# Performance work log

Measured on AMD Instinct MI355X. Metric: run time of the kernel, lower is better.

The kernel has to match this reference:

```python
import jax, jax.numpy as jnp
import numpy as np

H = 4          # heads (both HGTConv and MHA)
LN_EPS = 1e-5
ALPHA = 0.1


def _ln(x, g, b):
    m = x.mean(-1, keepdims=True)
    v = ((x - m) ** 2).mean(-1, keepdims=True)
    return (x - m) * jax.lax.rsqrt(v + LN_EPS) * g + b


def _kqv(x, Wk, bk, Wq, bq, Wv, bv, D):
    N = x.shape[0]
    k = (x @ Wk.T + bk).reshape(N, H, D)
    q = (x @ Wq.T + bq).reshape(N, H, D)
    v = (x @ Wv.T + bv).reshape(N, H, D)
    return k, q, v


def _hgt_edge(q_dst, k_src, v_src, a_rel, m_rel, p_rel, src, dst, n_dst):
    """PyG HGTConv message passing for one edge type: relation-transform,
    per-dst-node softmax, weighted scatter-sum."""
    D = q_dst.shape[-1]
    k = jnp.einsum('nhd,hde->nhe', k_src, a_rel)   # [N_src,H,D]
    v = jnp.einsum('nhd,hde->nhe', v_src, m_rel)
    logit = (q_dst[dst] * k[src]).sum(-1) * p_rel / np.sqrt(D)   # [E,H]
    mx = jax.ops.segment_max(logit, dst, num_segments=n_dst)
    e = jnp.exp(logit - mx[dst])
    s = jax.ops.segment_sum(e, dst, num_segments=n_dst)
    a = e / (s[dst] + 1e-16)
    return jax.ops.segment_sum(v[src] * a[..., None], dst, num_segments=n_dst)  # [N_dst,H,D]


def _hgt_out(agg, x, Wout, bout, skip):
    N, dim = x.shape
    o = jax.nn.gelu(agg.reshape(N, dim), approximate=False) @ Wout.T + bout
    a = jax.nn.sigmoid(skip)
    return a * o + (1.0 - a) * x


def _mha(x, Wi, bi, Wo, bo):
    # self-attention over all entities as a single sequence (batch=1)
    N, dim = x.shape
    D = dim // H
    q, k, v = jnp.split(x @ Wi.T + bi, 3, axis=-1)
    q = q.reshape(N, H, D).transpose(1, 0, 2)
    k = k.reshape(N, H, D).transpose(1, 0, 2)
    v = v.reshape(N, H, D).transpose(1, 0, 2)
    att = jax.nn.softmax(jnp.einsum('hnd,hmd->hnm', q, k) / np.sqrt(D), axis=-1)
    o = jnp.einsum('hnm,hmd->hnd', att, v).transpose(1, 0, 2).reshape(N, dim)
    return o @ Wo.T + bo


def _forward(x_entity, x_passage, query_emb,
             Wk_ent, bk_ent, Wq_ent, bq_ent, Wv_ent, bv_ent, Wout_ent, bout_ent, skip_ent,
             Wk_psg, bk_psg, Wq_psg, bq_psg, Wv_psg, bv_psg, Wout_psg, bout_psg, skip_psg,
             a_e2p, m_e2p, p_e2p, a_p2e, m_p2e, p_p2e,
             mha_in_w, mha_in_b, mha_out_w, mha_out_b,
             ln_ent_g, ln_ent_b, ln_psg_g, ln_psg_b,
             w1, b1, w2, b2,
             e2p_src, e2p_dst, p2e_src, p2e_dst):
    N_e, dim = x_entity.shape
    N_p = x_passage.shape[0]
    D = dim // H
    # ---- HGTConv ----
    k_e, q_e, v_e = _kqv(x_entity, Wk_ent, bk_ent, Wq_ent, bq_ent, Wv_ent, bv_ent, D)
    k_p, q_p, v_p = _kqv(x_passage, Wk_psg, bk_psg, Wq_psg, bq_psg, Wv_psg, bv_psg, D)
    agg_p = _hgt_edge(q_p, k_e, v_e, a_e2p, m_e2p, p_e2p, e2p_src, e2p_dst, N_p)
    agg_e = _hgt_edge(q_e, k_p, v_p, a_p2e, m_p2e, p_p2e, p2e_src, p2e_dst, N_e)
    h_ent = _hgt_out(agg_e, x_entity, Wout_ent, bout_ent, skip_ent)
    h_psg = _hgt_out(agg_p, x_passage, Wout_psg, bout_psg, skip_psg)
    # ---- global entity attention + residual mix + LN ----
    h_glob = _mha(h_ent, mha_in_w, mha_in_b, mha_out_w, mha_out_b)
    h_ent = _ln((1.0 - ALPHA) * h_ent + ALPHA * h_glob, ln_ent_g, ln_ent_b)
    # ---- gather-scale-scatter entity -> passage (kernel target) ----
    q = query_emb.reshape(-1)
    rel = jax.nn.sigmoid(h_ent @ q)                          # [N_e]
    w_ent = h_ent[e2p_src] * rel[e2p_src][:, None]           # gather + scale
    ctx = jax.ops.segment_sum(w_ent, e2p_dst, num_segments=N_p)  # scatter-add
    h_psg = _ln(h_psg + ctx, ln_psg_g, ln_psg_b)
    # ---- scoring head ----
    feats = jnp.concatenate([h_psg, jnp.broadcast_to(q, (N_p, dim))], axis=-1)
    scores = (jax.nn.relu(feats @ w1.T + b1) @ w2.T + b2).squeeze(-1)
    return scores


def setup_inputs() -> dict:
    key = jax.random.key(0)
    N_E, N_P, DIM, NE = 4096, 4096, 256, 262144
    D = DIM // H
    ks = iter(jax.random.split(key, 64))
    def rn(shape, s=1.0):
        return jax.random.normal(next(ks), shape, jnp.float32) * s
    w = 0.05
    inp = {
        'x_entity': rn((N_E, DIM)),
        'x_passage': rn((N_P, DIM)),
        'query_emb': rn((DIM,)),
    }
    for t in ('ent', 'psg'):
        inp['Wk_' + t] = rn((DIM, DIM), w); inp['bk_' + t] = jnp.zeros((DIM,))
        inp['Wq_' + t] = rn((DIM, DIM), w); inp['bq_' + t] = jnp.zeros((DIM,))
        inp['Wv_' + t] = rn((DIM, DIM), w); inp['bv_' + t] = jnp.zeros((DIM,))
        inp['Wout_' + t] = rn((DIM, DIM), w); inp['bout_' + t] = jnp.zeros((DIM,))
        inp['skip_' + t] = jnp.ones(())
    for e in ('e2p', 'p2e'):
        inp['a_' + e] = rn((H, D, D), w)
        inp['m_' + e] = rn((H, D, D), w)
        inp['p_' + e] = jnp.ones((H,))
    inp['mha_in_w'] = rn((3 * DIM, DIM), w); inp['mha_in_b'] = jnp.zeros((3 * DIM,))
    inp['mha_out_w'] = rn((DIM, DIM), w); inp['mha_out_b'] = jnp.zeros((DIM,))
    inp['ln_ent_g'] = jnp.ones((DIM,)); inp['ln_ent_b'] = jnp.zeros((DIM,))
    inp['ln_psg_g'] = jnp.ones((DIM,)); inp['ln_psg_b'] = jnp.zeros((DIM,))
    inp['w1'] = rn((DIM, 2 * DIM), w); inp['b1'] = jnp.zeros((DIM,))
    inp['w2'] = rn((1, DIM), w); inp['b2'] = jnp.zeros((1,))
    inp['e2p_src'] = jax.random.randint(next(ks), (NE,), 0, N_E, jnp.int32)
    inp['e2p_dst'] = jax.random.randint(next(ks), (NE,), 0, N_P, jnp.int32)
    inp['p2e_src'] = jax.random.randint(next(ks), (NE,), 0, N_P, jnp.int32)
    inp['p2e_dst'] = jax.random.randint(next(ks), (NE,), 0, N_E, jnp.int32)
    return inp


def reference(x_entity, x_passage, query_emb,
              Wk_ent, bk_ent, Wq_ent, bq_ent, Wv_ent, bv_ent, Wout_ent, bout_ent, skip_ent,
              Wk_psg, bk_psg, Wq_psg, bq_psg, Wv_psg, bv_psg, Wout_psg, bout_psg, skip_psg,
              a_e2p, m_e2p, p_e2p, a_p2e, m_p2e, p_p2e,
              mha_in_w, mha_in_b, mha_out_w, mha_out_b,
              ln_ent_g, ln_ent_b, ln_psg_g, ln_psg_b,
              w1, b1, w2, b2,
              e2p_src, e2p_dst, p2e_src, p2e_dst):
    return _forward(x_entity, x_passage, query_emb,
                    Wk_ent, bk_ent, Wq_ent, bq_ent, Wv_ent, bv_ent, Wout_ent, bout_ent, skip_ent,
                    Wk_psg, bk_psg, Wq_psg, bq_psg, Wv_psg, bv_psg, Wout_psg, bout_psg, skip_psg,
                    a_e2p, m_e2p, p_e2p, a_p2e, m_p2e, p_p2e,
                    mha_in_w, mha_in_b, mha_out_w, mha_out_b,
                    ln_ent_g, ln_ent_b, ln_psg_g, ln_psg_b,
                    w1, b1, w2, b2,
                    e2p_src, e2p_dst, p2e_src, p2e_dst)
```

## Files before the change

### kernel.cpp

```cpp
#include <hip/hip_runtime.h>
#include <hip/hip_bf16.h>
#include <math.h>

#define DIM 256
#define NHEAD 4
#define HD 64
#define MSPLIT 8

typedef __attribute__((ext_vector_type(8))) short short8b;
typedef __attribute__((ext_vector_type(4))) float f32x4;
typedef __attribute__((ext_vector_type(16))) float f32x16;
typedef __attribute__((ext_vector_type(2))) unsigned int uint2v;

union B8 { uint4 u; short8b v; };

__device__ __forceinline__ float sigmoidf_(float x) { return 1.0f / (1.0f + __expf(-x)); }
__device__ __forceinline__ float geluf_(float x) {
    return 0.5f * x * (1.0f + erff(x * 0.70710678118654752440f));
}
__device__ __forceinline__ float wave_sum64(float v) {
    v += __shfl_xor(v, 32); v += __shfl_xor(v, 16); v += __shfl_xor(v, 8);
    v += __shfl_xor(v, 4);  v += __shfl_xor(v, 2);  v += __shfl_xor(v, 1);
    return v;
}
__device__ __forceinline__ unsigned short f2bf(float f) {
    union { float f; unsigned int u; } a; a.f = f;
    unsigned int u = a.u;
    unsigned int r = (u + 0x7FFFu + ((u >> 16) & 1u)) >> 16;
    return (unsigned short)r;
}
__device__ __forceinline__ unsigned int cvtpk_(float lo, float hi) {
    unsigned int r;
    asm("v_cvt_pk_bf16_f32 %0, %1, %2" : "=v"(r) : "v"(lo), "v"(hi));
    return r;
}
__device__ __forceinline__ uint2v plswap_(unsigned int a, unsigned int b) {
    return __builtin_amdgcn_permlane32_swap(a, b, false, false);
}

template<int DO_GELU>
__launch_bounds__(256)
__global__ void cvt_bf16_kernel(const float* __restrict__ src,
                                unsigned short* __restrict__ dst, int n8)
{
    const int i = blockIdx.x * 256 + threadIdx.x;
    if (i >= n8) return;
    float4 a = reinterpret_cast<const float4*>(src)[2 * i];
    float4 b = reinterpret_cast<const float4*>(src)[2 * i + 1];
    if (DO_GELU) {
        a.x = geluf_(a.x); a.y = geluf_(a.y); a.z = geluf_(a.z); a.w = geluf_(a.w);
        b.x = geluf_(b.x); b.y = geluf_(b.y); b.z = geluf_(b.z); b.w = geluf_(b.w);
    }
    ushort4 lo = {f2bf(a.x), f2bf(a.y), f2bf(a.z), f2bf(a.w)};
    ushort4 hi = {f2bf(b.x), f2bf(b.y), f2bf(b.z), f2bf(b.w)};
    reinterpret_cast<ushort4*>(dst)[2 * i] = lo;
    reinterpret_cast<ushort4*>(dst)[2 * i + 1] = hi;
}

__launch_bounds__(256)
__global__ void cvt_w_kernel(const float* __restrict__ W0, const float* __restrict__ W1,
                             const float* __restrict__ W2, const float* __restrict__ W3,
                             const float* __restrict__ W4, const float* __restrict__ W5,
                             const float* __restrict__ W6, const float* __restrict__ W7,
                             const float* __restrict__ W8, const float* __restrict__ W9,
                             const float* __restrict__ W10, const float* __restrict__ W11,
                             unsigned short* __restrict__ arena)
{
    const float* s;
    switch (blockIdx.y) {
        case 0: s = W0; break;  case 1: s = W1; break;  case 2: s = W2; break;
        case 3: s = W3; break;  case 4: s = W4; break;  case 5: s = W5; break;
        case 6: s = W6; break;  case 7: s = W7; break;  case 8: s = W8; break;
        case 9: s = W9; break;  case 10: s = W10; break; default: s = W11; break;
    }
    const int i = blockIdx.x * 256 + threadIdx.x;
    unsigned short* dst = arena + (size_t)blockIdx.y * 65536;
    float4 a = reinterpret_cast<const float4*>(s)[2 * i];
    float4 b = reinterpret_cast<const float4*>(s)[2 * i + 1];
    ushort4 lo = {f2bf(a.x), f2bf(a.y), f2bf(a.z), f2bf(a.w)};
    ushort4 hi = {f2bf(b.x), f2bf(b.y), f2bf(b.z), f2bf(b.w)};
    reinterpret_cast<ushort4*>(dst)[2 * i] = lo;
    reinterpret_cast<ushort4*>(dst)[2 * i + 1] = hi;
}

template<int OUT_MODE, int WF32, int WBF>
__launch_bounds__(256)
__global__ void bgemm_kernel(const unsigned short* __restrict__ Abf,
                             const unsigned short* __restrict__ W0b,
                             const unsigned short* __restrict__ W1b,
                             const unsigned short* __restrict__ W2b,
                             const float* __restrict__ B0, const float* __restrict__ B1,
                             const float* __restrict__ B2,
                             float* __restrict__ C, int ldc,
                             unsigned short* __restrict__ Cbf, int ldcb,
                             const float* __restrict__ xres,
                             const float* __restrict__ skipv)
{
    const int t = threadIdx.x;
    const int lane = t & 63;
    const int wid = t >> 6;
    const int col16 = lane & 15;
    const int oct = lane >> 4;
    const int r0 = blockIdx.y * 64 + wid * 16;
    const int c0 = blockIdx.x * 64;
    const int widx = c0 >> 8;
    const unsigned short* W = (widx == 0) ? W0b : (widx == 1 ? W1b : W2b);
    const float* Bv = (widx == 0) ? B0 : (widx == 1 ? B1 : B2);
    const int cw = c0 & 255;

    const unsigned short* aptr = Abf + (size_t)(r0 + col16) * 256 + oct * 8;
    const unsigned short* wptr = W + (size_t)(cw + col16) * 256 + oct * 8;

    f32x4 acc0 = {0,0,0,0}, acc1 = {0,0,0,0}, acc2 = {0,0,0,0}, acc3 = {0,0,0,0};
#pragma unroll
    for (int k0 = 0; k0 < 256; k0 += 32) {
        B8 af, w0, w1, w2, w3;
        af.u = *reinterpret_cast<const uint4*>(aptr + k0);
        w0.u = *reinterpret_cast<const uint4*>(wptr + k0);
        w1.u = *reinterpret_cast<const uint4*>(wptr + k0 + 16 * 256);
        w2.u = *reinterpret_cast<const uint4*>(wptr + k0 + 32 * 256);
        w3.u = *reinterpret_cast<const uint4*>(wptr + k0 + 48 * 256);
        acc0 = __builtin_amdgcn_mfma_f32_16x16x32_bf16(af.v, w0.v, acc0, 0, 0, 0);
        acc1 = __builtin_amdgcn_mfma_f32_16x16x32_bf16(af.v, w1.v, acc1, 0, 0, 0);
        acc2 = __builtin_amdgcn_mfma_f32_16x16x32_bf16(af.v, w2.v, acc2, 0, 0, 0);
        acc3 = __builtin_amdgcn_mfma_f32_16x16x32_bf16(af.v, w3.v, acc3, 0, 0, 0);
    }

    float bias[4];
#pragma unroll
    for (int j = 0; j < 4; ++j) bias[j] = Bv[cw + j * 16 + col16];
    float sg = 0.f;
    if (OUT_MODE == 1) sg = sigmoidf_(skipv[0]);

    const float av[4][4] = {
        {acc0.x, acc0.y, acc0.z, acc0.w}, {acc1.x, acc1.y, acc1.z, acc1.w},
        {acc2.x, acc2.y, acc2.z, acc2.w}, {acc3.x, acc3.y, acc3.z, acc3.w}};
#pragma unroll
    for (int r = 0; r < 4; ++r) {
        const int row = r0 + oct * 4 + r;
#pragma unroll
        for (int j = 0; j < 4; ++j) {
            const int col = c0 + j * 16 + col16;
            float v = av[j][r] + bias[j];
            if (OUT_MODE == 1) {
                const float xv = xres[(size_t)row * ldc + col];
                v = sg * v + (1.f - sg) * xv;
            }
            if (WF32) C[(size_t)row * ldc + col] = v;
            if (WBF)  Cbf[(size_t)row * ldcb + col] = f2bf(v);
        }
    }
}

template<int IN_GELU, int OUT_MODE>
__launch_bounds__(256)
__global__ void gemm_kernel(const float* __restrict__ A, int lda,
                            const float* __restrict__ W0, const float* __restrict__ W1,
                            const float* __restrict__ W2, int ldw,
                            const float* __restrict__ B0, const float* __restrict__ B1,
                            const float* __restrict__ B2,
                            float* __restrict__ C, int ldc, int Kin,
                            float* __restrict__ scores,
                            const float* __restrict__ w2v,
                            const float* __restrict__ b2v)
{
    __shared__ float As[16][68];
    __shared__ float Ws[16][68];
    const int t = threadIdx.x;
    const int r0 = blockIdx.y * 64;
    const int c0 = blockIdx.x * 64;
    const int widx = c0 >> 8;
    const float* W  = (widx == 0) ? W0 : (widx == 1 ? W1 : W2);
    const float* Bv = (widx == 0) ? B0 : (widx == 1 ? B1 : B2);
    const int cw = c0 & 255;

    const int lrow = t >> 2;
    const int lk   = (t & 3) << 2;
    const int ty = t >> 4, tx = t & 15;

    const float* Aptr = A + (size_t)(r0 + lrow) * lda + lk;
    const float* Wptr = W + (size_t)(cw + lrow) * ldw + lk;

    float acc[4][4] = {};
    for (int k0 = 0; k0 < Kin; k0 += 16) {
        float4 av = *reinterpret_cast<const float4*>(Aptr + k0);
        float4 wv = *reinterpret_cast<const float4*>(Wptr + k0);
        if (IN_GELU) {
            av.x = geluf_(av.x); av.y = geluf_(av.y);
            av.z = geluf_(av.z); av.w = geluf_(av.w);
        }
        As[lk + 0][lrow] = av.x; As[lk + 1][lrow] = av.y;
        As[lk + 2][lrow] = av.z; As[lk + 3][lrow] = av.w;
        Ws[lk + 0][lrow] = wv.x; Ws[lk + 1][lrow] = wv.y;
        Ws[lk + 2][lrow] = wv.z; Ws[lk + 3][lrow] = wv.w;
        __syncthreads();
#pragma unroll
        for (int k = 0; k < 16; ++k) {
            const float4 a = *reinterpret_cast<const float4*>(&As[k][ty << 2]);
            const float4 b = *reinterpret_cast<const float4*>(&Ws[k][tx << 2]);
            const float ar[4] = {a.x, a.y, a.z, a.w};
            const float br[4] = {b.x, b.y, b.z, b.w};
#pragma unroll
            for (int i = 0; i < 4; ++i)
#pragma unroll
                for (int j = 0; j < 4; ++j)
                    acc[i][j] = fmaf(ar[i], br[j], acc[i][j]);
        }
        __syncthreads();
    }

    float bias[4];
#pragma unroll
    for (int j = 0; j < 4; ++j) bias[j] = Bv[cw + (tx << 2) + j];

    if (OUT_MODE == 0) {
#pragma unroll
        for (int i = 0; i < 4; ++i) {
            float4 st;
            st.x = acc[i][0] + bias[0]; st.y = acc[i][1] + bias[1];
            st.z = acc[i][2] + bias[2]; st.w = acc[i][3] + bias[3];
            *reinterpret_cast<float4*>(&C[(size_t)(r0 + (ty << 2) + i) * ldc + c0 + (tx << 2)]) = st;
        }
    } else {
        float wv[4];
#pragma unroll
        for (int j = 0; j < 4; ++j) wv[j] = w2v[c0 + (tx << 2) + j];
#pragma unroll
        for (int i = 0; i < 4; ++i) {
            float p = 0.f;
#pragma unroll
            for (int j = 0; j < 4; ++j)
                p = fmaf(fmaxf(acc[i][j] + bias[j], 0.f), wv[j], p);
            if (c0 == 0 && tx == 0) p += b2v[0];
            atomicAdd(&scores[r0 + (ty << 2) + i], p);
        }
    }
}

__launch_bounds__(256)
__global__ void rel_transform_kernel(const float* __restrict__ kin, int ldin,
                                     const float* __restrict__ arel,
                                     float* __restrict__ kout)
{
    __shared__ float Al[64][68];
    __shared__ float Kl[64][65];
    const int t = threadIdx.x;
    const int r0 = blockIdx.x * 64;
    const int h = blockIdx.y;
    const float* ah = arel + h * 4096;
    for (int i = t; i < 1024; i += 256) {
        const int rr = i >> 4, c4 = (i & 15) << 2;
        const float4 av = *reinterpret_cast<const float4*>(&ah[rr * 64 + c4]);
        *reinterpret_cast<float4*>(&Al[rr][c4]) = av;
        const float4 kv = *reinterpret_cast<const float4*>(&kin[(size_t)(r0 + rr) * ldin + h * 64 + c4]);
        Kl[rr][c4 + 0] = kv.x; Kl[rr][c4 + 1] = kv.y;
        Kl[rr][c4 + 2] = kv.z; Kl[rr][c4 + 3] = kv.w;
    }
    __syncthreads();
    const int r  = t & 63;
    const int e0 = (t >> 6) << 4;
    float acc[16] = {};
    for (int d = 0; d < 64; ++d) {
        const float kv = Kl[r][d];
#pragma unroll
        for (int u4 = 0; u4 < 4; ++u4) {
            const float4 a = *reinterpret_cast<const float4*>(&Al[d][e0 + (u4 << 2)]);
            acc[u4 * 4 + 0] = fmaf(kv, a.x, acc[u4 * 4 + 0]);
            acc[u4 * 4 + 1] = fmaf(kv, a.y, acc[u4 * 4 + 1]);
            acc[u4 * 4 + 2] = fmaf(kv, a.z, acc[u4 * 4 + 2]);
            acc[u4 * 4 + 3] = fmaf(kv, a.w, acc[u4 * 4 + 3]);
        }
    }
#pragma unroll
    for (int u4 = 0; u4 < 4; ++u4) {
        float4 st = {acc[u4 * 4 + 0], acc[u4 * 4 + 1], acc[u4 * 4 + 2], acc[u4 * 4 + 3]};
        *reinterpret_cast<float4*>(&kout[(size_t)(r0 + r) * 256 + h * 64 + e0 + (u4 << 2)]) = st;
    }
}

__global__ void edge_count_kernel(const int* __restrict__ dst, int* __restrict__ cnt, int E)
{
    const int i = blockIdx.x * 256 + threadIdx.x;
    if (i < E) atomicAdd(&cnt[dst[i]], 1);
}

__launch_bounds__(1024)
__global__ void scan_kernel(const int* __restrict__ cnt, int* __restrict__ indptr,
                            int* __restrict__ cursor)
{
    __shared__ int sh[1024];
    const int t = threadIdx.x;
    const int4 v = *reinterpret_cast<const int4*>(&cnt[t << 2]);
    const int sum = v.x + v.y + v.z + v.w;
    sh[t] = sum;
    __syncthreads();
    for (int off = 1; off < 1024; off <<= 1) {
        int x = 0;
        if (t >= off) x = sh[t - off];
        __syncthreads();
        if (t >= off) sh[t] += x;
        __syncthreads();
    }
    int run = sh[t] - sum;
    const int base = t << 2;
    if (t == 0) indptr[0] = 0;
    cursor[base + 0] = run; run += v.x; indptr[base + 1] = run;
    cursor[base + 1] = run; run += v.y; indptr[base + 2] = run;
    cursor[base + 2] = run; run += v.z; indptr[base + 3] = run;
    cursor[base + 3] = run; run += v.w; indptr[base + 4] = run;
}

__global__ void edge_scatter_kernel(const int* __restrict__ src, const int* __restrict__ dst,
                                    int* __restrict__ cursor, int* __restrict__ ssrc, int E)
{
    const int i = blockIdx.x * 256 + threadIdx.x;
    if (i < E) {
        const int p = atomicAdd(&cursor[dst[i]], 1);
        ssrc[p] = src[i];
    }
}

__launch_bounds__(256)
__global__ void hgt_attn_kernel(const float* __restrict__ qdst,
                                const float* __restrict__ kt,
                                const float* __restrict__ vt,
                                const float* __restrict__ prel,
                                const int* __restrict__ indptr,
                                const int* __restrict__ ssrc,
                                float* __restrict__ agg)
{
    const int n = blockIdx.x * 4 + (threadIdx.x >> 6);
    const int lane = threadIdx.x & 63;
    const int h = lane >> 4;
    const int d4 = (lane & 15) << 2;
    const float4 q = *reinterpret_cast<const float4*>(&qdst[(size_t)n * 768 + h * 64 + d4]);
    const float ps = prel[h] * 0.125f;
    const int e0 = indptr[n], e1 = indptr[n + 1];
    float m = -1e30f, s = 0.f;
    float4 acc = {0.f, 0.f, 0.f, 0.f};
    float4 kc = {0.f, 0.f, 0.f, 0.f}, vc = {0.f, 0.f, 0.f, 0.f};
    if (e0 < e1) {
        const int sr0 = ssrc[e0];
        kc = *reinterpret_cast<const float4*>(&kt[(size_t)sr0 * 256 + h * 64 + d4]);
        vc = *reinterpret_cast<const float4*>(&vt[(size_t)sr0 * 256 + h * 64 + d4]);
    }
    for (int e = e0; e < e1; ++e) {
        const float4 k = kc, v = vc;
        const int nsr = ssrc[(e + 1 < e1) ? (e + 1) : e];
        kc = *reinterpret_cast<const float4*>(&kt[(size_t)nsr * 256 + h * 64 + d4]);
        vc = *reinterpret_cast<const float4*>(&vt[(size_t)nsr * 256 + h * 64 + d4]);
        float d = q.x * k.x + q.y * k.y + q.z * k.z + q.w * k.w;
        d += __shfl_xor(d, 1); d += __shfl_xor(d, 2);
        d += __shfl_xor(d, 4); d += __shfl_xor(d, 8);
        const float logit = d * ps;
        const float mn = fmaxf(m, logit);
        const float f = __expf(m - mn);
        const float p = __expf(logit - mn);
        s = s * f + p;
        acc.x = acc.x * f + p * v.x;
        acc.y = acc.y * f + p * v.y;
        acc.z = acc.z * f + p * v.z;
        acc.w = acc.w * f + p * v.w;
        m = mn;
    }
    const float inv = 1.f / (s + 1e-16f);
    float4 st = {acc.x * inv, acc.y * inv, acc.z * inv, acc.w * inv};
    *reinterpret_cast<float4*>(&agg[(size_t)n * 256 + h * 64 + d4]) = st;
}

__launch_bounds__(256)
__global__ void vtrans_kernel(const unsigned short* __restrict__ qkv_bf,
                              unsigned short* __restrict__ vt, int N)
{
    __shared__ unsigned short tile[64][66];
    const int t = threadIdx.x;
    const int k0 = blockIdx.x * 64;
    const int h = blockIdx.y;
    {
        const int key = t >> 2;
        const int d0 = (t & 3) << 4;
        const unsigned short* src = qkv_bf + (size_t)(k0 + key) * 768 + 512 + h * 64 + d0;
        const uint4 a = *reinterpret_cast<const uint4*>(src);
        const uint4 b = *reinterpret_cast<const uint4*>(src + 8);
        const unsigned int w_[8] = {a.x, a.y, a.z, a.w, b.x, b.y, b.z, b.w};
#pragma unroll
        for (int j = 0; j < 8; ++j) {
            tile[d0 + 2 * j][key]     = (unsigned short)(w_[j] & 0xffff);
            tile[d0 + 2 * j + 1][key] = (unsigned short)(w_[j] >> 16);
        }
    }
    __syncthreads();
    {
        const int d = t >> 2;
        const int kk = (t & 3) << 4;
        unsigned int o_[8];
#pragma unroll
        for (int j = 0; j < 8; ++j)
            o_[j] = (unsigned int)tile[d][kk + 2 * j] | ((unsigned int)tile[d][kk + 2 * j + 1] << 16);
        unsigned short* dstp = vt + (size_t)(h * 64 + d) * N + k0 + kk;
        uint4 s0 = {o_[0], o_[1], o_[2], o_[3]};
        uint4 s1 = {o_[4], o_[5], o_[6], o_[7]};
        *reinterpret_cast<uint4*>(dstp) = s0;
        *reinterpret_cast<uint4*>(dstp + 8) = s1;
    }
}

__launch_bounds__(256)
__global__ void mha_mfma_kernel(const unsigned short* __restrict__ qkv_bf,
                                const unsigned short* __restrict__ vt_bf,
                                float* __restrict__ opart,
                                float* __restrict__ mpart,
                                float* __restrict__ lpart,
                                int N)
{
    const int lane = threadIdx.x & 63;
    const int l31 = lane & 31;
    const int hi = lane >> 5;
    const int gw = blockIdx.x * 4 + (threadIdx.x >> 6);
    const int split = gw & (MSPLIT - 1);
    const int gq = gw / MSPLIT;
    const int h = gq >> 7;
    const int qt = gq & 127;
    const int q0 = qt * 32;
    const int kbeg = split * (N / MSPLIT);
    const int kend = kbeg + (N / MSPLIT);

    B8 qf0, qf1, qf2, qf3;
    {
        const unsigned short* qp = qkv_bf + (size_t)(q0 + l31) * 768 + h * 64 + hi * 8;
        qf0.u = *reinterpret_cast<const uint4*>(qp);
        qf1.u = *reinterpret_cast<const uint4*>(qp + 16);
        qf2.u = *reinterpret_cast<const uint4*>(qp + 32);
        qf3.u = *reinterpret_cast<const uint4*>(qp + 48);
    }

    f32x16 o0, o1;
#pragma unroll
    for (int i = 0; i < 16; ++i) { o0[i] = 0.f; o1[i] = 0.f; }
    float m_run = -1e30f, l_run = 0.f;

    const unsigned short* kbase = qkv_bf + 256 + h * 64 + hi * 8;
    const unsigned short* vbase = vt_bf + (size_t)(h * 64 + l31) * N + hi * 8;

    for (int ck = kbeg; ck < kend; ck += 32) {
        const unsigned short* kp = kbase + (size_t)(ck + l31) * 768;
        B8 kf0, kf1, kf2, kf3;
        kf0.u = *reinterpret_cast<const uint4*>(kp);
        kf1.u = *reinterpret_cast<const uint4*>(kp + 16);
        kf2.u = *reinterpret_cast<const uint4*>(kp + 32);
        kf3.u = *reinterpret_cast<const uint4*>(kp + 48);
        const unsigned short* vp = vbase + ck;
        B8 vf00, vf01, vf10, vf11;
        vf00.u = *reinterpret_cast<const uint4*>(vp);
        vf01.u = *reinterpret_cast<const uint4*>(vp + 16);
        vf10.u = *reinterpret_cast<const uint4*>(vp + (size_t)32 * N);
        vf11.u = *reinterpret_cast<const uint4*>(vp + (size_t)32 * N + 16);

        f32x16 s;
#pragma unroll
        for (int i = 0; i < 16; ++i) s[i] = 0.f;
        s = __builtin_amdgcn_mfma_f32_32x32x16_bf16(kf0.v, qf0.v, s, 0, 0, 0);
        s = __builtin_amdgcn_mfma_f32_32x32x16_bf16(kf1.v, qf1.v, s, 0, 0, 0);
        s = __builtin_amdgcn_mfma_f32_32x32x16_bf16(kf2.v, qf2.v, s, 0, 0, 0);
        s = __builtin_amdgcn_mfma_f32_32x32x16_bf16(kf3.v, qf3.v, s, 0, 0, 0);

        float mx = s[0];
#pragma unroll
        for (int i = 1; i < 16; ++i) mx = fmaxf(mx, s[i]);
        mx *= 0.125f;
        {
            uint2v mr = plswap_(__float_as_uint(mx), __float_as_uint(mx));
            mx = fmaxf(__uint_as_float(mr[0]), __uint_as_float(mr[1]));
        }
        const float mnew = fmaxf(m_run, mx);
        const float f = __expf(m_run - mnew);
        m_run = mnew;

        float p[16];
        float sum = 0.f;
#pragma unroll
        for (int i = 0; i < 16; ++i) {
            p[i] = __expf(fmaf(s[i], 0.125f, -mnew));
            sum += p[i];
        }
        l_run = l_run * f + sum;
        o0 *= f;
        o1 *= f;

        unsigned int w0 = cvtpk_(p[0], p[1]),  w1 = cvtpk_(p[2], p[3]);
        unsigned int w2 = cvtpk_(p[4], p[5]),  w3 = cvtpk_(p[6], p[7]);
        unsigned int w4 = cvtpk_(p[8], p[9]),  w5 = cvtpk_(p[10], p[11]);
        unsigned int w6 = cvtpk_(p[12], p[13]), w7 = cvtpk_(p[14], p[15]);
        uint2v r02 = plswap_(w0, w2);
        uint2v r13 = plswap_(w1, w3);
        uint2v r46 = plswap_(w4, w6);
        uint2v r57 = plswap_(w5, w7);
        B8 pb0, pb1;
        pb0.u = (uint4){r02[0], r13[0], r02[1], r13[1]};
        pb1.u = (uint4){r46[0], r57[0], r46[1], r57[1]};

        o0 = __builtin_amdgcn_mfma_f32_32x32x16_bf16(vf00.v, pb0.v, o0, 0, 0, 0);
        o0 = __builtin_amdgcn_mfma_f32_32x32x16_bf16(vf01.v, pb1.v, o0, 0, 0, 0);
        o1 = __builtin_amdgcn_mfma_f32_32x32x16_bf16(vf10.v, pb0.v, o1, 0, 0, 0);
        o1 = __builtin_amdgcn_mfma_f32_32x32x16_bf16(vf11.v, pb1.v, o1, 0, 0, 0);
    }

    {
        uint2v lr = plswap_(__float_as_uint(l_run), __float_as_uint(l_run));
        l_run = __uint_as_float(lr[0]) + __uint_as_float(lr[1]);
    }

    float* op = opart + ((size_t)split * N + q0 + l31) * 256 + h * 64 + 4 * hi;
#pragma unroll
    for (int u = 0; u < 4; ++u) {
        float4 s0_ = {o0[4 * u + 0], o0[4 * u + 1], o0[4 * u + 2], o0[4 * u + 3]};
        *reinterpret_cast<float4*>(op + 8 * u) = s0_;
        float4 s1_ = {o1[4 * u + 0], o1[4 * u + 1], o1[4 * u + 2], o1[4 * u + 3]};
        *reinterpret_cast<float4*>(op + 32 + 8 * u) = s1_;
    }
    if (hi == 0) {
        mpart[((size_t)split * NHEAD + h) * N + q0 + l31] = m_run;
        lpart[((size_t)split * NHEAD + h) * N + q0 + l31] = l_run;
    }
}

__launch_bounds__(256)
__global__ void mha_combine_kernel(const float* __restrict__ opart,
                                   const float* __restrict__ mpart,
                                   const float* __restrict__ lpart,
                                   unsigned short* __restrict__ outpb, int N)
{
    const int q = blockIdx.x;
    const int c = threadIdx.x;
    const int h = c >> 6;
    const size_t base = (size_t)q * 256 + c;
    float m[MSPLIT], l[MSPLIT];
    float M = -1e30f;
#pragma unroll
    for (int s = 0; s < MSPLIT; ++s) {
        m[s] = mpart[(size_t)(s * NHEAD + h) * N + q];
        l[s] = lpart[(size_t)(s * NHEAD + h) * N + q];
        M = fmaxf(M, m[s]);
    }
    float L = 0.f, o = 0.f;
#pragma unroll
    for (int s = 0; s < MSPLIT; ++s) {
        const float w = __expf(m[s] - M);
        L += w * l[s];
        o = fmaf(w, opart[(size_t)s * N * 256 + base], o);
    }
    outpb[base] = f2bf(o / L);
}

__launch_bounds__(256)
__global__ void mix_ln_rel_kernel(float* __restrict__ he, const float* __restrict__ hg,
                                  const float* __restrict__ g, const float* __restrict__ b,
                                  const float* __restrict__ q, float* __restrict__ rel)
{
    const int row = (blockIdx.x * 256 + threadIdx.x) >> 6;
    const int lane = threadIdx.x & 63;
    const float4 a = *reinterpret_cast<const float4*>(&he[(size_t)row * 256 + (lane << 2)]);
    const float4 c = *reinterpret_cast<const float4*>(&hg[(size_t)row * 256 + (lane << 2)]);
    float4 v;
    v.x = 0.9f * a.x + 0.1f * c.x; v.y = 0.9f * a.y + 0.1f * c.y;
    v.z = 0.9f * a.z + 0.1f * c.z; v.w = 0.9f * a.w + 0.1f * c.w;
    const float mean = wave_sum64(v.x + v.y + v.z + v.w) * (1.f / 256.f);
    float4 d = {v.x - mean, v.y - mean, v.z - mean, v.w - mean};
    const float var = wave_sum64(d.x * d.x + d.y * d.y + d.z * d.z + d.w * d.w) * (1.f / 256.f);
    const float rs = rsqrtf(var + 1e-5f);
    const float4 gg = *reinterpret_cast<const float4*>(&g[lane << 2]);
    const float4 bb = *reinterpret_cast<const float4*>(&b[lane << 2]);
    float4 y = {d.x * rs * gg.x + bb.x, d.y * rs * gg.y + bb.y,
                d.z * rs * gg.z + bb.z, d.w * rs * gg.w + bb.w};
    *reinterpret_cast<float4*>(&he[(size_t)row * 256 + (lane << 2)]) = y;
    const float4 qq = *reinterpret_cast<const float4*>(&q[lane << 2]);
    const float dq = wave_sum64(y.x * qq.x + y.y * qq.y + y.z * qq.z + y.w * qq.w);
    if (lane == 0) rel[row] = sigmoidf_(dq);
}

__launch_bounds__(256)
__global__ void ctx_gather_kernel(const float* __restrict__ he, const float* __restrict__ rel,
                                  const int* __restrict__ indptr, const int* __restrict__ ssrc,
                                  float* __restrict__ ctx)
{
    const int gw = (blockIdx.x * 256 + threadIdx.x) >> 6;
    const int lane = threadIdx.x & 63;
    const int p = gw >> 2, qt = gw & 3;
    const int e0 = indptr[p], e1 = indptr[p + 1];
    float acc = 0.f;
    for (int e = e0; e < e1; ++e) {
        const int sr = ssrc[e];
        acc = fmaf(he[(size_t)sr * 256 + qt * 64 + lane], rel[sr], acc);
    }
    ctx[(size_t)p * 256 + qt * 64 + lane] = acc;
}

__launch_bounds__(256)
__global__ void psg_ln_kernel(float* __restrict__ hp, const float* __restrict__ ctx,
                              const float* __restrict__ g, const float* __restrict__ b)
{
    const int row = (blockIdx.x * 256 + threadIdx.x) >> 6;
    const int lane = threadIdx.x & 63;
    const float4 a = *reinterpret_cast<const float4*>(&hp[(size_t)row * 256 + (lane << 2)]);
    const float4 c = *reinterpret_cast<const float4*>(&ctx[(size_t)row * 256 + (lane << 2)]);
    float4 v = {a.x + c.x, a.y + c.y, a.z + c.z, a.w + c.w};
    const float mean = wave_sum64(v.x + v.y + v.z + v.w) * (1.f / 256.f);
    float4 d = {v.x - mean, v.y - mean, v.z - mean, v.w - mean};
    const float var = wave_sum64(d.x * d.x + d.y * d.y + d.z * d.z + d.w * d.w) * (1.f / 256.f);
    const float rs = rsqrtf(var + 1e-5f);
    const float4 gg = *reinterpret_cast<const float4*>(&g[lane << 2]);
    const float4 bb = *reinterpret_cast<const float4*>(&b[lane << 2]);
    float4 y = {d.x * rs * gg.x + bb.x, d.y * rs * gg.y + bb.y,
                d.z * rs * gg.z + bb.z, d.w * rs * gg.w + bb.w};
    *reinterpret_cast<float4*>(&hp[(size_t)row * 256 + (lane << 2)]) = y;
}

__global__ void qterm_kernel(const float* __restrict__ w1, const float* __restrict__ b1,
                             const float* __restrict__ q, float* __restrict__ qterm)
{
    __shared__ float qs[256];
    const int t = threadIdx.x;
    qs[t] = q[t];
    __syncthreads();
    float s = b1[t];
    for (int k = 0; k < 256; ++k) s = fmaf(w1[(size_t)t * 512 + 256 + k], qs[k], s);
    qterm[t] = s;
}

extern "C" void kernel_launch(void* const* d_in, const int* in_sizes, int n_in,
                              void* d_out, int out_size, void* d_ws, size_t ws_size,
                              hipStream_t stream)
{
    const float* x_ent = (const float*)d_in[0];
    const float* x_psg = (const float*)d_in[1];
    const float* q_emb = (const float*)d_in[2];
    const float* Wk_e = (const float*)d_in[3];  const float* bk_e = (const float*)d_in[4];
    const float* Wq_e = (const float*)d_in[5];  const float* bq_e = (const float*)d_in[6];
    const float* Wv_e = (const float*)d_in[7];  const float* bv_e = (const float*)d_in[8];
    const float* Wo_e = (const float*)d_in[9];  const float* bo_e = (const float*)d_in[10];
    const float* sk_e = (const float*)d_in[11];
    const float* Wk_p = (const float*)d_in[12]; const float* bk_p = (const float*)d_in[13];
    const float* Wq_p = (const float*)d_in[14]; const float* bq_p = (const float*)d_in[15];
    const float* Wv_p = (const float*)d_in[16]; const float* bv_p = (const float*)d_in[17];
    const float* Wo_p = (const float*)d_in[18]; const float* bo_p = (const float*)d_in[19];
    const float* sk_p = (const float*)d_in[20];
    const float* a_e2p = (const float*)d_in[21];
    const float* m_e2p = (const float*)d_in[22];
    const float* p_e2p = (const float*)d_in[23];
    const float* a_p2e = (const float*)d_in[24];
    const float* m_p2e = (const float*)d_in[25];
    const float* p_p2e = (const float*)d_in[26];
    const float* Wmi = (const float*)d_in[27];  const float* bmi = (const float*)d_in[28];
    const float* Wmo = (const float*)d_in[29];  const float* bmo = (const float*)d_in[30];
    const float* lng_e = (const float*)d_in[31]; const float* lnb_e = (const float*)d_in[32];
    const float* lng_p = (const float*)d_in[33]; const float* lnb_p = (const float*)d_in[34];
    const float* w1 = (const float*)d_in[35];   const float* b1 = (const float*)d_in[36];
    const float* w2 = (const float*)d_in[37];   const float* b2 = (const float*)d_in[38];
    const int* e2p_src = (const int*)d_in[39];
    const int* e2p_dst = (const int*)d_in[40];
    const int* p2e_src = (const int*)d_in[41];
    const int* p2e_dst = (const int*)d_in[42];

    const int NE = in_sizes[0] / DIM;
    const int NP = in_sizes[1] / DIM;
    const int E  = in_sizes[39];
    float* scores = (float*)d_out;

    char* wp = (char*)d_ws;
    auto alloc = [&](size_t bytes) -> void* {
        void* r = (void*)wp;
        wp += (bytes + 255) & ~(size_t)255;
        return r;
    };
    float* kqv_e = (float*)alloc((size_t)NE * 768 * 4);
    float* kqv_p = (float*)alloc((size_t)NP * 768 * 4);
    float* kt_e  = (float*)alloc((size_t)NE * 256 * 4);
    float* vt_e  = (float*)alloc((size_t)NE * 256 * 4);
    float* kt_p  = (float*)alloc((size_t)NP * 256 * 4);
    float* vt_p  = (float*)alloc((size_t)NP * 256 * 4);
    float* agg_p = (float*)alloc((size_t)NP * 256 * 4);
    float* agg_e = (float*)alloc((size_t)NE * 256 * 4);
    float* h_ent = (float*)alloc((size_t)NE * 256 * 4);
    float* h_psg = (float*)alloc((size_t)NP * 256 * 4);
    float* h_glob= (float*)alloc((size_t)NE * 256 * 4);
    float* relv  = (float*)alloc((size_t)NE * 4);
    float* ctxb  = (float*)alloc((size_t)NP * 256 * 4);
    float* qterm = (float*)alloc(256 * 4);
    unsigned short* warena  = (unsigned short*)alloc((size_t)12 * 65536 * 2);
    unsigned short* xe_bf   = (unsigned short*)alloc((size_t)NE * 256 * 2);
    unsigned short* xp_bf   = (unsigned short*)alloc((size_t)NP * 256 * 2);
    unsigned short* ge_bf   = (unsigned short*)alloc((size_t)NE * 256 * 2);
    unsigned short* gp_bf   = (unsigned short*)alloc((size_t)NP * 256 * 2);
    unsigned short* hent_bf = (unsigned short*)alloc((size_t)NE * 256 * 2);
    unsigned short* atto_bf = (unsigned short*)alloc((size_t)NE * 256 * 2);
    unsigned short* qkv_bf  = (unsigned short*)alloc((size_t)NE * 768 * 2);
    unsigned short* vt_bf   = (unsigned short*)alloc((size_t)256 * NE * 2);
    float* mpart = (float*)alloc((size_t)MSPLIT * NHEAD * NE * 4);
    float* lpart = (float*)alloc((size_t)MSPLIT * NHEAD * NE * 4);
    float* opart = kqv_e;
    int* cnt_a = (int*)alloc((size_t)NP * 4);
    int* cur_a = (int*)alloc((size_t)NP * 4);
    int* ip_a  = (int*)alloc((size_t)(NP + 1) * 4);
    int* ss_a  = (int*)alloc((size_t)E * 4);
    int* cnt_b = (int*)alloc((size_t)NE * 4);
    int* cur_b = (int*)alloc((size_t)NE * 4);
    int* ip_b  = (int*)alloc((size_t)(NE + 1) * 4);
    int* ss_b  = (int*)alloc((size_t)E * 4);

    hipMemsetAsync(cnt_a, 0, (size_t)NP * 4, stream);
    hipMemsetAsync(cnt_b, 0, (size_t)NE * 4, stream);
    hipMemsetAsync(d_out, 0, (size_t)out_size * 4, stream);

    cvt_w_kernel<<<dim3(32, 12), 256, 0, stream>>>(
        Wk_e, Wq_e, Wv_e, Wo_e, Wk_p, Wq_p, Wv_p, Wo_p,
        Wmi, Wmi + 65536, Wmi + 131072, Wmo, warena);
    cvt_bf16_kernel<0><<<NE * 256 / 2048, 256, 0, stream>>>(x_ent, xe_bf, NE * 32);
    cvt_bf16_kernel<0><<<NP * 256 / 2048, 256, 0, stream>>>(x_psg, xp_bf, NP * 32);

    const int eb = (E + 255) / 256;
    edge_count_kernel<<<eb, 256, 0, stream>>>(e2p_dst, cnt_a, E);
    edge_count_kernel<<<eb, 256, 0, stream>>>(p2e_dst, cnt_b, E);
    scan_kernel<<<1, 1024, 0, stream>>>(cnt_a, ip_a, cur_a);
    scan_kernel<<<1, 1024, 0, stream>>>(cnt_b, ip_b, cur_b);
    edge_scatter_kernel<<<eb, 256, 0, stream>>>(e2p_src, e2p_dst, cur_a, ss_a, E);
    edge_scatter_kernel<<<eb, 256, 0, stream>>>(p2e_src, p2e_dst, cur_b, ss_b, E);

    bgemm_kernel<0,1,0><<<dim3(12, NE / 64), 256, 0, stream>>>(
        xe_bf, warena, warena + 65536, warena + 131072, bk_e, bq_e, bv_e,
        kqv_e, 768, nullptr, 0, nullptr, nullptr);
    bgemm_kernel<0,1,0><<<dim3(12, NP / 64), 256, 0, stream>>>(
        xp_bf, warena + 4*65536, warena + 5*65536, warena + 6*65536, bk_p, bq_p, bv_p,
        kqv_p, 768, nullptr, 0, nullptr, nullptr);

    rel_transform_kernel<<<dim3(NE / 64, NHEAD), 256, 0, stream>>>(kqv_e + 0,   768, a_e2p, kt_e);
    rel_transform_kernel<<<dim3(NE / 64, NHEAD), 256, 0, stream>>>(kqv_e + 512, 768, m_e2p, vt_e);
    rel_transform_kernel<<<dim3(NP / 64, NHEAD), 256, 0, stream>>>(kqv_p + 0,   768, a_p2e, kt_p);
    rel_transform_kernel<<<dim3(NP / 64, NHEAD), 256, 0, stream>>>(kqv_p + 512, 768, m_p2e, vt_p);

    hgt_attn_kernel<<<NP / 4, 256, 0, stream>>>(kqv_p + 256, kt_e, vt_e, p_e2p, ip_a, ss_a, agg_p);
    hgt_attn_kernel<<<NE / 4, 256, 0, stream>>>(kqv_e + 256, kt_p, vt_p, p_p2e, ip_b, ss_b, agg_e);

    cvt_bf16_kernel<1><<<NE * 256 / 2048, 256, 0, stream>>>(agg_e, ge_bf, NE * 32);
    cvt_bf16_kernel<1><<<NP * 256 / 2048, 256, 0, stream>>>(agg_p, gp_bf, NP * 32);
    bgemm_kernel<1,1,1><<<dim3(4, NE / 64), 256, 0, stream>>>(
        ge_bf, warena + 3*65536, warena + 3*65536, warena + 3*65536, bo_e, bo_e, bo_e,
        h_ent, 256, hent_bf, 256, x_ent, sk_e);
    bgemm_kernel<1,1,0><<<dim3(4, NP / 64), 256, 0, stream>>>(
        gp_bf, warena + 7*65536, warena + 7*65536, warena + 7*65536, bo_p, bo_p, bo_p,
        h_psg, 256, nullptr, 0, x_psg, sk_p);

    bgemm_kernel<0,0,1><<<dim3(12, NE / 64), 256, 0, stream>>>(
        hent_bf, warena + 8*65536, warena + 9*65536, warena + 10*65536,
        bmi, bmi + 256, bmi + 512,
        nullptr, 0, qkv_bf, 768, nullptr, nullptr);
    vtrans_kernel<<<dim3(NE / 64, NHEAD), 256, 0, stream>>>(qkv_bf, vt_bf, NE);
    mha_mfma_kernel<<<NHEAD * (NE / 32) * MSPLIT / 4, 256, 0, stream>>>(
        qkv_bf, vt_bf, opart, mpart, lpart, NE);
    mha_combine_kernel<<<NE, 256, 0, stream>>>(opart, mpart, lpart, atto_bf, NE);
    bgemm_kernel<0,1,0><<<dim3(4, NE / 64), 256, 0, stream>>>(
        atto_bf, warena + 11*65536, warena + 11*65536, warena + 11*65536, bmo, bmo, bmo,
        h_glob, 256, nullptr, 0, nullptr, nullptr);

    mix_ln_rel_kernel<<<NE / 4, 256, 0, stream>>>(h_ent, h_glob, lng_e, lnb_e, q_emb, relv);

    ctx_gather_kernel<<<NP, 256, 0, stream>>>(h_ent, relv, ip_a, ss_a, ctxb);
    psg_ln_kernel<<<NP / 4, 256, 0, stream>>>(h_psg, ctxb, lng_p, lnb_p);

    qterm_kernel<<<1, 256, 0, stream>>>(w1, b1, q_emb, qterm);
    gemm_kernel<0,2><<<dim3(4, NP / 64), 256, 0, stream>>>(
        h_psg, 256, w1, w1, w1, 512, qterm, qterm, qterm,
        nullptr, 256, 256, scores, w2, b2);
}
```

Measured before the change: 673.7 us.

## Process 64 keys per flash-attention iteration and skip rescale when max is stable

The MHA flash-attention inner loop now handles two 32-key blocks per iteration, interleaving independent MFMA chains for the two score tiles and the two output halves to hide MFMA latency and amortize the softmax reduction. It also adds a lazy rescale: the running max and output rescaling are only updated when some lane's new max exceeds the running max by more than 8, which avoids exp and multiply work on most iterations. This raises register pressure from doubled K/V fragments, assumes the key range is a multiple of 64, and lets exponentials grow up to e^8 before rescaling.

```diff
diff --git a/kernel.cpp b/kernel.cpp
--- a/kernel.cpp
+++ b/kernel.cpp
@@ -442,67 +442,105 @@
     const unsigned short* kbase = qkv_bf + 256 + h * 64 + hi * 8;
     const unsigned short* vbase = vt_bf + (size_t)(h * 64 + l31) * N + hi * 8;
 
-    for (int ck = kbeg; ck < kend; ck += 32) {
-        const unsigned short* kp = kbase + (size_t)(ck + l31) * 768;
-        B8 kf0, kf1, kf2, kf3;
-        kf0.u = *reinterpret_cast<const uint4*>(kp);
-        kf1.u = *reinterpret_cast<const uint4*>(kp + 16);
-        kf2.u = *reinterpret_cast<const uint4*>(kp + 32);
-        kf3.u = *reinterpret_cast<const uint4*>(kp + 48);
-        const unsigned short* vp = vbase + ck;
-        B8 vf00, vf01, vf10, vf11;
-        vf00.u = *reinterpret_cast<const uint4*>(vp);
-        vf01.u = *reinterpret_cast<const uint4*>(vp + 16);
-        vf10.u = *reinterpret_cast<const uint4*>(vp + (size_t)32 * N);
-        vf11.u = *reinterpret_cast<const uint4*>(vp + (size_t)32 * N + 16);
-
-        f32x16 s;
-#pragma unroll
-        for (int i = 0; i < 16; ++i) s[i] = 0.f;
-        s = __builtin_amdgcn_mfma_f32_32x32x16_bf16(kf0.v, qf0.v, s, 0, 0, 0);
-        s = __builtin_amdgcn_mfma_f32_32x32x16_bf16(kf1.v, qf1.v, s, 0, 0, 0);
-        s = __builtin_amdgcn_mfma_f32_32x32x16_bf16(kf2.v, qf2.v, s, 0, 0, 0);
-        s = __builtin_amdgcn_mfma_f32_32x32x16_bf16(kf3.v, qf3.v, s, 0, 0, 0);
-
-        float mx = s[0];
-#pragma unroll
-        for (int i = 1; i < 16; ++i) mx = fmaxf(mx, s[i]);
+    for (int ck = kbeg; ck < kend; ck += 64) {
+        const unsigned short* kpA = kbase + (size_t)(ck + l31) * 768;
+        const unsigned short* kpB = kbase + (size_t)(ck + 32 + l31) * 768;
+        B8 ka0, ka1, ka2, ka3, kb0, kb1, kb2, kb3;
+        ka0.u = *reinterpret_cast<const uint4*>(kpA);
+        ka1.u = *reinterpret_cast<const uint4*>(kpA + 16);
+        ka2.u = *reinterpret_cast<const uint4*>(kpA + 32);
+        ka3.u = *reinterpret_cast<const uint4*>(kpA + 48);
+        kb0.u = *reinterpret_cast<const uint4*>(kpB);
+        kb1.u = *reinterpret_cast<const uint4*>(kpB + 16);
+        kb2.u = *reinterpret_cast<const uint4*>(kpB + 32);
+        kb3.u = *reinterpret_cast<const uint4*>(kpB + 48);
+        const unsigned short* vp0 = vbase + ck;
+        const unsigned short* vp1 = vbase + (size_t)32 * N + ck;
+        B8 va0, va1, va2, va3, vb0, vb1, vb2, vb3;
+        va0.u = *reinterpret_cast<const uint4*>(vp0);
+        va1.u = *reinterpret_cast<const uint4*>(vp0 + 16);
+        va2.u = *reinterpret_cast<const uint4*>(vp0 + 32);
+        va3.u = *reinterpret_cast<const uint4*>(vp0 + 48);
+        vb0.u = *reinterpret_cast<const uint4*>(vp1);
+        vb1.u = *reinterpret_cast<const uint4*>(vp1 + 16);
+        vb2.u = *reinterpret_cast<const uint4*>(vp1 + 32);
+        vb3.u = *reinterpret_cast<const uint4*>(vp1 + 48);
+
+        f32x16 sA, sB;
+#pragma unroll
+        for (int i = 0; i < 16; ++i) { sA[i] = 0.f; sB[i] = 0.f; }
+        sA = __builtin_amdgcn_mfma_f32_32x32x16_bf16(ka0.v, qf0.v, sA, 0, 0, 0);
+        sB = __builtin_amdgcn_mfma_f32_32x32x16_bf16(kb0.v, qf0.v, sB, 0, 0, 0);
+        sA = __builtin_amdgcn_mfma_f32_32x32x16_bf16(ka1.v, qf1.v, sA, 0, 0, 0);
+        sB = __builtin_amdgcn_mfma_f32_32x32x16_bf16(kb1.v, qf1.v, sB, 0, 0, 0);
+        sA = __builtin_amdgcn_mfma_f32_32x32x16_bf16(ka2.v, qf2.v, sA, 0, 0, 0);
+        sB = __builtin_amdgcn_mfma_f32_32x32x16_bf16(kb2.v, qf2.v, sB, 0, 0, 0);
+        sA = __builtin_amdgcn_mfma_f32_32x32x16_bf16(ka3.v, qf3.v, sA, 0, 0, 0);
+        sB = __builtin_amdgcn_mfma_f32_32x32x16_bf16(kb3.v, qf3.v, sB, 0, 0, 0);
+
+        float mx = sA[0];
+#pragma unroll
+        for (int i = 1; i < 16; ++i) mx = fmaxf(mx, sA[i]);
+#pragma unroll
+        for (int i = 0; i < 16; ++i) mx = fmaxf(mx, sB[i]);
         mx *= 0.125f;
         {
             uint2v mr = plswap_(__float_as_uint(mx), __float_as_uint(mx));
             mx = fmaxf(__uint_as_float(mr[0]), __uint_as_float(mr[1]));
         }
-        const float mnew = fmaxf(m_run, mx);
-        const float f = __expf(m_run - mnew);
-        m_run = mnew;
-
-        float p[16];
+        if (!__all(mx <= m_run + 8.0f)) {
+            const float mnew = fmaxf(m_run, mx);
+            const float f = __expf(m_run - mnew);
+            l_run *= f;
+            o0 *= f;
+            o1 *= f;
+            m_run = mnew;
+        }
+
+        float p[32];
         float sum = 0.f;
 #pragma unroll
         for (int i = 0; i < 16; ++i) {
-            p[i] = __expf(fmaf(s[i], 0.125f, -mnew));
+            p[i] = __expf(fmaf(sA[i], 0.125f, -m_run));
             sum += p[i];
         }
-        l_run = l_run * f + sum;
-        o0 *= f;
-        o1 *= f;
-
-        unsigned int w0 = cvtpk_(p[0], p[1]),  w1 = cvtpk_(p[2], p[3]);
-        unsigned int w2 = cvtpk_(p[4], p[5]),  w3 = cvtpk_(p[6], p[7]);
-        unsigned int w4 = cvtpk_(p[8], p[9]),  w5 = cvtpk_(p[10], p[11]);
+#pragma unroll
+        for (int i = 0; i < 16; ++i) {
+            p[16 + i] = __expf(fmaf(sB[i], 0.125f, -m_run));
+            sum += p[16 + i];
+        }
+        l_run += sum;
+
+        unsigned int w0 = cvtpk_(p[0], p[1]),   w1 = cvtpk_(p[2], p[3]);
+        unsigned int w2 = cvtpk_(p[4], p[5]),   w3 = cvtpk_(p[6], p[7]);
+        unsigned int w4 = cvtpk_(p[8], p[9]),   w5 = cvtpk_(p[10], p[11]);
         unsigned int w6 = cvtpk_(p[12], p[13]), w7 = cvtpk_(p[14], p[15]);
         uint2v r02 = plswap_(w0, w2);
         uint2v r13 = plswap_(w1, w3);
         uint2v r46 = plswap_(w4, w6);
         uint2v r57 = plswap_(w5, w7);
-        B8 pb0, pb1;
+        B8 pb0, pb1, pb2, pb3;
         pb0.u = (uint4){r02[0], r13[0], r02[1], r13[1]};
         pb1.u = (uint4){r46[0], r57[0], r46[1], r57[1]};
-
-        o0 = __builtin_amdgcn_mfma_f32_32x32x16_bf16(vf00.v, pb0.v, o0, 0, 0, 0);
-        o0 = __builtin_amdgcn_mfma_f32_32x32x16_bf16(vf01.v, pb1.v, o0, 0, 0, 0);
-        o1 = __builtin_amdgcn_mfma_f32_32x32x16_bf16(vf10.v, pb0.v, o1, 0, 0, 0);
-        o1 = __builtin_amdgcn_mfma_f32_32x32x16_bf16(vf11.v, pb1.v, o1, 0, 0, 0);
+        unsigned int x0 = cvtpk_(p[16], p[17]), x1 = cvtpk_(p[18], p[19]);
+        unsigned int x2 = cvtpk_(p[20], p[21]), x3 = cvtpk_(p[22], p[23]);
+        unsigned int x4 = cvtpk_(p[24], p[25]), x5 = cvtpk_(p[26], p[27]);
+        unsigned int x6 = cvtpk_(p[28], p[29]), x7 = cvtpk_(p[30], p[31]);
+        uint2v q02 = plswap_(x0, x2);
+        uint2v q13 = plswap_(x1, x3);
+        uint2v q46 = plswap_(x4, x6);
+        uint2v q57 = plswap_(x5, x7);
+        pb2.u = (uint4){q02[0], q13[0], q02[1], q13[1]};
+        pb3.u = (uint4){q46[0], q57[0], q46[1], q57[1]};
+
+        o0 = __builtin_amdgcn_mfma_f32_32x32x16_bf16(va0.v, pb0.v, o0, 0, 0, 0);
+        o1 = __builtin_amdgcn_mfma_f32_32x32x16_bf16(vb0.v, pb0.v, o1, 0, 0, 0);
+        o0 = __builtin_amdgcn_mfma_f32_32x32x16_bf16(va1.v, pb1.v, o0, 0, 0, 0);
+        o1 = __builtin_amdgcn_mfma_f32_32x32x16_bf16(vb1.v, pb1.v, o1, 0, 0, 0);
+        o0 = __builtin_amdgcn_mfma_f32_32x32x16_bf16(va2.v, pb2.v, o0, 0, 0, 0);
+        o1 = __builtin_amdgcn_mfma_f32_32x32x16_bf16(vb2.v, pb2.v, o1, 0, 0, 0);
+        o0 = __builtin_amdgcn_mfma_f32_32x32x16_bf16(va3.v, pb3.v, o0, 0, 0, 0);
+        o1 = __builtin_amdgcn_mfma_f32_32x32x16_bf16(vb3.v, pb3.v, o1, 0, 0, 0);
     }
 
     {
```

Result: no change. 667.0 us (-1.0%).
